# Kernel optimization log

Measured on AMD Instinct MI355X. Metric: run time of the kernel, lower is better.

## Reference

```python
import jax, jax.numpy as jnp
import numpy as np

T, D, H, HD = 2048, 2048, 16, 128
ROPE_BASE = 10000.0
NEG = jnp.float32(-1e30)


def rms_norm(x):
    # F.rms_norm(x, (x.size(-1),)) with default eps = dtype eps
    eps = jnp.finfo(x.dtype).eps
    return x * jax.lax.rsqrt(jnp.mean(x * x, axis=-1, keepdims=True) + eps)


def rotary(x):
    # x: [1, T, H, hd]; half-split rotation as in Rotary.forward
    hd = x.shape[-1]
    inv_freq = (1.0 / ROPE_BASE) ** (jnp.arange(0, hd, 2, dtype=jnp.float32) / hd)
    t = jnp.arange(x.shape[1], dtype=jnp.float32)
    freqs = jnp.outer(t, inv_freq)                      # [T, hd/2]
    cos = jnp.cos(freqs)[None, :, None, :]
    sin = jnp.sin(freqs)[None, :, None, :]
    x1, x2 = jnp.split(x, 2, axis=-1)
    return jnp.concatenate([x1 * cos + x2 * sin, -x1 * sin + x2 * cos], axis=-1)


def setup_inputs() -> dict:
    key = jax.random.key(0)
    ks = jax.random.split(key, 10)
    w = lambda k, shape: jax.random.normal(k, shape, jnp.float32) * 0.02
    return {
        "x":  jax.random.normal(ks[0], (1, T, D), jnp.float32),
        "vi": jax.random.normal(ks[1], (1, T, H, HD), jnp.float32),
        "x0": jax.random.normal(ks[2], (1, T, D), jnp.float32),
        "wq": w(ks[3], (D, D)),
        "wk": w(ks[4], (D, D)),
        "wv": w(ks[5], (D, D)),
        "wo": w(ks[6], (D, D)),
        "lamb": jnp.float32(0.5),
        "lambdas": jnp.array([1.0, 0.0], jnp.float32),
        "w_fc": w(ks[7], (4 * D, D)),
        "w_proj": w(ks[8], (D, 4 * D)),
    }


def reference(x, vi, x0, wq, wk, wv, wo, lamb, lambdas, w_fc, w_proj):
    # Block: residual blend with initial embedding x0
    xb = lambdas[0] * x + lambdas[1] * x0
    xn = rms_norm(xb)

    # --- CausalSelfAttention ---
    q = (xn @ wq.T).reshape(1, T, H, HD)
    k = (xn @ wk.T).reshape(1, T, H, HD)
    v = (xn @ wv.T).reshape(1, T, H, HD)
    v = (1.0 - lamb) * v + lamb * vi                     # value-embedding blend
    q = rotary(rms_norm(q))
    k = rotary(rms_norm(k))

    scale = 1.0 / jnp.sqrt(jnp.float32(HD))              # flex_attention default scale
    scores = jnp.einsum('bqhd,bkhd->bhqk', q, k) * scale # [1,H,T,T]
    causal = jnp.tril(jnp.ones((T, T), bool))
    scores = jnp.where(causal[None, None], scores, NEG)
    attn = jax.nn.softmax(scores, axis=-1)
    y = jnp.einsum('bhqk,bkhd->bqhd', attn, v).reshape(1, T, D)
    a = y @ wo.T                                         # attention output REPLACES x (no residual)

    # --- MLP with squared ReLU ---
    h = rms_norm(a) @ w_fc.T
    h = jnp.square(jax.nn.relu(h))
    out = a + h @ w_proj.T
    return out
```

## Files before the change

### kernel.cpp

```cpp
#include <hip/hip_runtime.h>
#include <hip/hip_bf16.h>

typedef __bf16 bf16;
typedef __bf16 bf16x8 __attribute__((ext_vector_type(8)));
typedef float f32x4 __attribute__((ext_vector_type(4)));
typedef unsigned int u32x4 __attribute__((ext_vector_type(4)));

#define DD 2048
#define DD2 4194304ull
#define G9_LDS 131072

__device__ __forceinline__ void glds16(const void* g, void* l) {
  __builtin_amdgcn_global_load_lds((const __attribute__((address_space(1))) void*)g,
                                   (__attribute__((address_space(3))) void*)l, 16, 0, 0);
}

__device__ __forceinline__ f32x4 mfma16(bf16x8 a, bf16x8 b, f32x4 c) {
  return __builtin_amdgcn_mfma_f32_16x16x32_bf16(a, b, c, 0, 0, 0);
}

__device__ __forceinline__ unsigned pk2(float lo, float hi) {
  unsigned short a = __builtin_bit_cast(unsigned short, (bf16)lo);
  unsigned short b = __builtin_bit_cast(unsigned short, (bf16)hi);
  return (unsigned)a | ((unsigned)b << 16);
}

__global__ __launch_bounds__(256) void cvt_seg(const float* __restrict__ s0, const float* __restrict__ s1,
                                               const float* __restrict__ s2, const float* __restrict__ s3,
                                               bf16* __restrict__ dst, int seglog, size_t total) {
  size_t i = ((size_t)blockIdx.x * 256 + threadIdx.x) * 16;
  const size_t stride = (size_t)gridDim.x * 256 * 16;
  for (; i < total; i += stride) {
    int seg = (int)(i >> seglog);
    const float* src = (seg == 0) ? s0 : (seg == 1) ? s1 : (seg == 2) ? s2 : s3;
    size_t loc = i - ((size_t)seg << seglog);
    float4 a0 = *(const float4*)(src + loc);
    float4 a1 = *(const float4*)(src + loc + 4);
    float4 a2 = *(const float4*)(src + loc + 8);
    float4 a3 = *(const float4*)(src + loc + 12);
    bf16x8 o0, o1;
    o0[0] = (bf16)a0.x; o0[1] = (bf16)a0.y; o0[2] = (bf16)a0.z; o0[3] = (bf16)a0.w;
    o0[4] = (bf16)a1.x; o0[5] = (bf16)a1.y; o0[6] = (bf16)a1.z; o0[7] = (bf16)a1.w;
    o1[0] = (bf16)a2.x; o1[1] = (bf16)a2.y; o1[2] = (bf16)a2.z; o1[3] = (bf16)a2.w;
    o1[4] = (bf16)a3.x; o1[5] = (bf16)a3.y; o1[6] = (bf16)a3.z; o1[7] = (bf16)a3.w;
    *(bf16x8*)(dst + i) = o0;
    *(bf16x8*)(dst + i + 8) = o1;
  }
}

template<bool BLEND>
__global__ __launch_bounds__(256) void prenorm_k(const float* __restrict__ x, const float* __restrict__ x0,
                                                 const float* __restrict__ lambdas, bf16* __restrict__ out) {
  const int t = blockIdx.x, tid = threadIdx.x;
  const float4* xr = (const float4*)(x + (size_t)t * DD);
  float4 a0 = xr[2 * tid], a1 = xr[2 * tid + 1];
  float v[8] = {a0.x, a0.y, a0.z, a0.w, a1.x, a1.y, a1.z, a1.w};
  if (BLEND) {
    const float l0 = lambdas[0], l1 = lambdas[1];
    const float4* yr = (const float4*)(x0 + (size_t)t * DD);
    float4 b0 = yr[2 * tid], b1 = yr[2 * tid + 1];
    float w[8] = {b0.x, b0.y, b0.z, b0.w, b1.x, b1.y, b1.z, b1.w};
#pragma unroll
    for (int i = 0; i < 8; ++i) v[i] = l0 * v[i] + l1 * w[i];
  }
  float ss = 0.f;
#pragma unroll
  for (int i = 0; i < 8; ++i) ss += v[i] * v[i];
#pragma unroll
  for (int off = 1; off < 64; off <<= 1) ss += __shfl_xor(ss, off, 64);
  __shared__ float red[4];
  const int wid = tid >> 6;
  if ((tid & 63) == 0) red[wid] = ss;
  __syncthreads();
  ss = red[0] + red[1] + red[2] + red[3];
  const float sc = rsqrtf(ss * (1.0f / DD) + 1.1920928955078125e-07f);
  bf16x8 o;
#pragma unroll
  for (int i = 0; i < 8; ++i) o[i] = (bf16)(v[i] * sc);
  *(bf16x8*)(out + (size_t)t * DD + tid * 8) = o;
}

__global__ __launch_bounds__(256) void rope_k(bf16* __restrict__ qg, bf16* __restrict__ kg) {
  const int tid = threadIdx.x, lane = tid & 63, wid = tid >> 6;
  const int p = blockIdx.x * 4 + wid;
  bf16* base = ((p >> 15) ? kg : qg);
  const int t = (p >> 4) & 2047, hh = p & 15;
  base += (size_t)t * DD + hh * 128;
  float x1 = (float)base[lane], x2 = (float)base[lane + 64];
  float ss = x1 * x1 + x2 * x2;
#pragma unroll
  for (int off = 1; off < 64; off <<= 1) ss += __shfl_xor(ss, off, 64);
  const float sc = rsqrtf(ss * (1.0f / 128.0f) + 1.1920928955078125e-07f);
  x1 *= sc; x2 *= sc;
  const float fr = (float)t * exp2f((float)lane * (-13.287712379549449f / 64.0f));
  const float s = sinf(fr), c = cosf(fr);
  base[lane]      = (bf16)(x1 * c + x2 * s);
  base[lane + 64] = (bf16)(-x1 * s + x2 * c);
}

__global__ __launch_bounds__(256) void vt_k(const bf16* __restrict__ v, bf16* __restrict__ vt) {
  __shared__ alignas(16) bf16 tile[16 * 128];
  const int tb = blockIdx.x, hb = blockIdx.y, tid = threadIdx.x;
  glds16(v + (size_t)(tb * 16 + (tid >> 4)) * DD + hb * 128 + (tid & 15) * 8, tile + tid * 8);
  __syncthreads();
  const int d_l = tid & 127, tc = tid >> 7;
  bf16x8 o;
#pragma unroll
  for (int i = 0; i < 8; ++i) o[i] = tile[(tc * 8 + i) * 128 + d_l];
  *(bf16x8*)(vt + (size_t)(hb * 128 + d_l) * DD + tb * 16 + tc * 8) = o;
}

__device__ __forceinline__ void g9_stageA(const bf16* A, int Kstride, int row0, int k0,
                                          bf16* buf, int hm, int tid) {
#pragma unroll
  for (int i = 0; i < 2; ++i) {
    int e = tid + i * 512;
    int prl = e >> 3, slot = e & 7;
    int wm = prl >> 6, r63 = prl & 63;
    glds16(A + (size_t)(row0 + wm * 128 + hm * 64 + r63) * Kstride + k0 + ((slot ^ (prl & 7)) * 8),
           buf + hm * 8192 + e * 8);
  }
}
__device__ __forceinline__ void g9_stageB(const bf16* B, int Kstride, int col0, int k0,
                                          bf16* buf, int hn, int tid) {
#pragma unroll
  for (int i = 0; i < 2; ++i) {
    int e = tid + i * 512;
    int pbl = e >> 3, slot = e & 7;
    int wn = pbl >> 5, q = pbl & 31;
    glds16(B + (size_t)(col0 + wn * 64 + hn * 32 + q) * Kstride + k0 + ((slot ^ (pbl & 7)) * 8),
           buf + 16384 + hn * 8192 + e * 8);
  }
}

__device__ __forceinline__ void gemm9_core(const bf16* __restrict__ A, const bf16* __restrict__ B,
                                           int Kstride, int Klen, int row0, int col0,
                                           bf16* smem, f32x4 (&acc)[8][4]) {
  const int tid = threadIdx.x, lane = tid & 63, wid = tid >> 6;
  const int wm = wid >> 2, wn = wid & 3;
  const int l15 = lane & 15, g = lane >> 4;
  const int sw = l15 & 7;
  const int NT = Klen >> 6;
  g9_stageA(A, Kstride, row0, 0, smem, 0, tid);
  g9_stageB(B, Kstride, col0, 0, smem, 0, tid);
  g9_stageB(B, Kstride, col0, 0, smem, 1, tid);
  g9_stageA(A, Kstride, row0, 0, smem, 1, tid);
  g9_stageA(A, Kstride, row0, 64, smem + 32768, 0, tid);
  g9_stageB(B, Kstride, col0, 64, smem + 32768, 0, tid);
  asm volatile("s_waitcnt vmcnt(8)" ::: "memory");
  __builtin_amdgcn_s_barrier();

  bf16x8 a[4][2], b0[2][2], b1[2][2];
  for (int t = 0; t < NT; ++t) {
    bf16* cb = smem + (t & 1) * 32768;
    bf16* nb = smem + ((t + 1) & 1) * 32768;
    const bool s1 = (t + 1) < NT, s2 = (t + 2) < NT;
#pragma unroll
    for (int mm = 0; mm < 4; ++mm)
#pragma unroll
      for (int ks = 0; ks < 2; ++ks)
        a[mm][ks] = *(const bf16x8*)(cb + (wm * 64 + mm * 16 + l15) * 64 + (((ks * 4 + g) ^ sw) * 8));
#pragma unroll
    for (int nn = 0; nn < 2; ++nn)
#pragma unroll
      for (int ks = 0; ks < 2; ++ks)
        b0[nn][ks] = *(const bf16x8*)(cb + 16384 + (wn * 32 + nn * 16 + l15) * 64 + (((ks * 4 + g) ^ sw) * 8));
    if (s1) { g9_stageB(B, Kstride, col0, (t + 1) << 6, nb, 1, tid);
              g9_stageA(A, Kstride, row0, (t + 1) << 6, nb, 1, tid);
              asm volatile("s_waitcnt vmcnt(8)" ::: "memory"); }
    else    { asm volatile("s_waitcnt vmcnt(0)" ::: "memory"); }
    __builtin_amdgcn_s_barrier();
    __builtin_amdgcn_s_setprio(1);
#pragma unroll
    for (int mm = 0; mm < 4; ++mm)
#pragma unroll
      for (int nn = 0; nn < 2; ++nn)
#pragma unroll
        for (int ks = 0; ks < 2; ++ks)
          acc[mm][nn] = mfma16(a[mm][ks], b0[nn][ks], acc[mm][nn]);
    __builtin_amdgcn_s_setprio(0);
#pragma unroll
    for (int nn = 0; nn < 2; ++nn)
#pragma unroll
      for (int ks = 0; ks < 2; ++ks)
        b1[nn][ks] = *(const bf16x8*)(cb + 16384 + 8192 + (wn * 32 + nn * 16 + l15) * 64 + (((ks * 4 + g) ^ sw) * 8));
    __builtin_amdgcn_s_barrier();
    __builtin_amdgcn_s_setprio(1);
#pragma unroll
    for (int mm = 0; mm < 4; ++mm)
#pragma unroll
      for (int nn = 0; nn < 2; ++nn)
#pragma unroll
        for (int ks = 0; ks < 2; ++ks)
          acc[mm][2 + nn] = mfma16(a[mm][ks], b1[nn][ks], acc[mm][2 + nn]);
    __builtin_amdgcn_s_setprio(0);
#pragma unroll
    for (int mm = 0; mm < 4; ++mm)
#pragma unroll
      for (int ks = 0; ks < 2; ++ks)
        a[mm][ks] = *(const bf16x8*)(cb + 8192 + (wm * 64 + mm * 16 + l15) * 64 + (((ks * 4 + g) ^ sw) * 8));
    __builtin_amdgcn_s_barrier();
    __builtin_amdgcn_s_setprio(1);
#pragma unroll
    for (int mm = 0; mm < 4; ++mm)
#pragma unroll
      for (int nn = 0; nn < 2; ++nn)
#pragma unroll
        for (int ks = 0; ks < 2; ++ks)
          acc[4 + mm][nn] = mfma16(a[mm][ks], b0[nn][ks], acc[4 + mm][nn]);
    __builtin_amdgcn_s_setprio(0);
    if (s2) { g9_stageA(A, Kstride, row0, (t + 2) << 6, cb, 0, tid);
              g9_stageB(B, Kstride, col0, (t + 2) << 6, cb, 0, tid);
              asm volatile("s_waitcnt vmcnt(8)" ::: "memory"); }
    else if (s1) { asm volatile("s_waitcnt vmcnt(4)" ::: "memory"); }
    __builtin_amdgcn_s_barrier();
    __builtin_amdgcn_s_setprio(1);
#pragma unroll
    for (int mm = 0; mm < 4; ++mm)
#pragma unroll
      for (int nn = 0; nn < 2; ++nn)
#pragma unroll
        for (int ks = 0; ks < 2; ++ks)
          acc[4 + mm][2 + nn] = mfma16(a[mm][ks], b1[nn][ks], acc[4 + mm][2 + nn]);
    __builtin_amdgcn_s_setprio(0);
  }
}

#define GEMM9_EPI(STMT)                                                        \
  { const int lane_ = threadIdx.x & 63, wid_ = threadIdx.x >> 6;               \
    const int l15_ = lane_ & 15, g_ = lane_ >> 4;                              \
    const int wm_ = wid_ >> 2, wn_ = wid_ & 3;                                 \
    _Pragma("unroll") for (int m = 0; m < 8; ++m)                              \
    _Pragma("unroll") for (int n = 0; n < 4; ++n)                              \
    _Pragma("unroll") for (int j = 0; j < 4; ++j) {                            \
      int grow = row0 + wm_ * 128 + (m >> 2) * 64 + (m & 3) * 16 + g_ * 4 + j; \
      int gcol = col0 + wn_ * 64 + (n >> 1) * 32 + (n & 1) * 16 + l15_;        \
      float vacc = acc[m][n][j];                                               \
      STMT; } }

__global__ __launch_bounds__(512, 1) void gemm9_qkv(const bf16* __restrict__ A,
    const bf16* __restrict__ Wq, const bf16* __restrict__ Wk, const bf16* __restrict__ Wv,
    bf16* __restrict__ oq, bf16* __restrict__ ok, bf16* __restrict__ ov,
    const float* __restrict__ vi, const float* __restrict__ lambp) {
  extern __shared__ bf16 smem9[];
  const int z = blockIdx.z;
  const bf16* B = (z == 0) ? Wq : (z == 1) ? Wk : Wv;
  bf16* out = (z == 0) ? oq : (z == 1) ? ok : ov;
  const int row0 = blockIdx.y * 256, col0 = blockIdx.x * 256;
  f32x4 acc[8][4] = {};
  gemm9_core(A, B, DD, DD, row0, col0, smem9, acc);
  if (z < 2) {
    GEMM9_EPI( out[(size_t)grow * DD + gcol] = (bf16)vacc; )
  } else {
    const float lam = *lambp;
    GEMM9_EPI( out[(size_t)grow * DD + gcol] =
                 (bf16)((1.0f - lam) * vacc + lam * vi[(size_t)grow * DD + gcol]); )
  }
}

__global__ __launch_bounds__(512, 1) void gemm9_part(const bf16* __restrict__ A, const bf16* __restrict__ B,
                                                     float* __restrict__ o1, float* __restrict__ o2,
                                                     int zsw, int N, int Kstride, int Klen) {
  extern __shared__ bf16 smem9[];
  const int row0 = blockIdx.y * 256, col0 = blockIdx.x * 256;
  const int z = blockIdx.z, kofs = z * Klen;
  float* out = (z < zsw) ? (o1 + (size_t)z * DD2) : (o2 + (size_t)(z - zsw) * DD2);
  f32x4 acc[8][4] = {};
  gemm9_core(A + kofs, B + kofs, Kstride, Klen, row0, col0, smem9, acc);
  GEMM9_EPI( out[(size_t)grow * N + gcol] = vacc; )
}

__global__ __launch_bounds__(512, 1) void gemm9_relu(const bf16* __restrict__ A, const bf16* __restrict__ B,
                                                     bf16* __restrict__ out, int N, int Kstride, int Klen) {
  extern __shared__ bf16 smem9[];
  const int row0 = blockIdx.y * 256, col0 = blockIdx.x * 256;
  f32x4 acc[8][4] = {};
  gemm9_core(A, B, Kstride, Klen, row0, col0, smem9, acc);
  GEMM9_EPI( float r = fmaxf(vacc, 0.f); out[(size_t)grow * N + gcol] = (bf16)(r * r); )
}

__global__ __launch_bounds__(256) void wo_red_prenorm(const float* __restrict__ pa, const float* __restrict__ pb,
                                                      float* __restrict__ a_f, bf16* __restrict__ an) {
  const int t = blockIdx.x, tid = threadIdx.x;
  const size_t base = (size_t)t * DD + tid * 8;
  float v[8];
#pragma unroll
  for (int h = 0; h < 2; ++h) {
    size_t i = base + h * 4;
    float4 r0 = *(const float4*)(pa + i);
    float4 r1 = *(const float4*)(pa + DD2 + i);
    float4 r2 = *(const float4*)(pb + i);
    float4 r3 = *(const float4*)(pb + DD2 + i);
    v[h*4+0] = r0.x + r1.x + r2.x + r3.x;
    v[h*4+1] = r0.y + r1.y + r2.y + r3.y;
    v[h*4+2] = r0.z + r1.z + r2.z + r3.z;
    v[h*4+3] = r0.w + r1.w + r2.w + r3.w;
  }
  *(float4*)(a_f + base)     = make_float4(v[0], v[1], v[2], v[3]);
  *(float4*)(a_f + base + 4) = make_float4(v[4], v[5], v[6], v[7]);
  float ss = 0.f;
#pragma unroll
  for (int i = 0; i < 8; ++i) ss += v[i] * v[i];
#pragma unroll
  for (int off = 1; off < 64; off <<= 1) ss += __shfl_xor(ss, off, 64);
  __shared__ float red[4];
  if ((tid & 63) == 0) red[tid >> 6] = ss;
  __syncthreads();
  ss = red[0] + red[1] + red[2] + red[3];
  const float sc = rsqrtf(ss * (1.0f / DD) + 1.1920928955078125e-07f);
  bf16x8 o;
#pragma unroll
  for (int i = 0; i < 8; ++i) o[i] = (bf16)(v[i] * sc);
  *(bf16x8*)(an + base) = o;
}

__global__ __launch_bounds__(256) void proj_red(const float* __restrict__ pa, const float* __restrict__ pw,
                                                const float* __restrict__ a_f, float* __restrict__ out) {
  const size_t base = ((size_t)blockIdx.x * 256 + threadIdx.x) * 8;
#pragma unroll
  for (int h = 0; h < 2; ++h) {
    size_t i = base + h * 4;
    float4 r = *(const float4*)(a_f + i);
    float4 u = *(const float4*)(pa + i);
    float4 w = *(const float4*)(pa + DD2 + i);
    float4 z = *(const float4*)(pa + 2 * DD2 + i);
    float4 y = *(const float4*)(pw + i);
    *(float4*)(out + i) = make_float4(r.x + u.x + w.x + z.x + y.x,
                                      r.y + u.y + w.y + z.y + y.y,
                                      r.z + u.z + w.z + z.z + y.z,
                                      r.w + u.w + w.w + z.w + y.w);
  }
}

__device__ __forceinline__ void att_stageK(const bf16* kg, int h, int kt, bf16* dst, int tid) {
#pragma unroll
  for (int r = 0; r < 2; ++r) {
    int e = tid + r * 256, row = e >> 4, slot = e & 15;
    glds16(kg + (size_t)(kt * 32 + row) * DD + h * 128 + ((slot ^ (row & 7)) * 8), dst + e * 8);
  }
}
__device__ __forceinline__ void att_stageV(const bf16* vtg, int h, int kt, bf16* dst, int tid) {
#pragma unroll
  for (int r = 0; r < 2; ++r) {
    int e = tid + r * 256, d = e >> 2, slot = e & 3;
    glds16(vtg + (size_t)(h * 128 + d) * DD + kt * 32 + ((slot ^ ((d >> 1) & 3)) * 8), dst + e * 8);
  }
}

__global__ __launch_bounds__(256) void attn_k(const bf16* __restrict__ qg, const bf16* __restrict__ kg,
                                              const bf16* __restrict__ vtg, bf16* __restrict__ yg) {
  __shared__ alignas(16) bf16 Ks[3][32 * 128];
  __shared__ alignas(16) bf16 Vt[3][128 * 32];
  const int h = blockIdx.y, qb = 31 - blockIdx.x;
  const int tid = threadIdx.x, lane = tid & 63, wid = tid >> 6;
  const int l15 = lane & 15, g = lane >> 4, swl = l15 & 7;
  const int qrow = qb * 64 + wid * 16;
  const float scale = 0.08838834764831845f;
  bf16x8 aQ[4];
  {
    const bf16* qp = qg + (size_t)(qrow + l15) * DD + h * 128 + g * 8;
#pragma unroll
    for (int kc = 0; kc < 4; ++kc) aQ[kc] = *(const bf16x8*)(qp + kc * 32);
  }
  f32x4 acc[8] = {};
  float lsum = 0.f;
  const int nkt = qb * 2 + 2;
  att_stageK(kg, h, 0, Ks[0], tid);
  att_stageV(vtg, h, 0, Vt[0], tid);
  att_stageK(kg, h, 1, Ks[1], tid);
  att_stageV(vtg, h, 1, Vt[1], tid);
  asm volatile("s_waitcnt vmcnt(4)" ::: "memory");
  __builtin_amdgcn_s_barrier();
  int cur = 0;
  for (int kt = 0; kt < nkt; ++kt) {
    const int kbase = kt * 32;
    const int nb = (cur >= 1) ? cur - 1 : 2;
    bf16x8 kf0[4], kf1[4];
#pragma unroll
    for (int kc = 0; kc < 4; ++kc) {
      kf0[kc] = *(const bf16x8*)(Ks[cur] + l15 * 128 + (((kc * 4 + g) ^ swl) * 8));
      kf1[kc] = *(const bf16x8*)(Ks[cur] + (16 + l15) * 128 + (((kc * 4 + g) ^ swl) * 8));
    }
    if (kt + 2 < nkt) { att_stageK(kg, h, kt + 2, Ks[nb], tid);
                        att_stageV(vtg, h, kt + 2, Vt[nb], tid); }
    f32x4 S0 = {}, S1 = {};
#pragma unroll
    for (int kc = 0; kc < 4; ++kc) {
      S0 = mfma16(kf0[kc], aQ[kc], S0);
      S1 = mfma16(kf1[kc], aQ[kc], S1);
    }
    const int q = qrow + l15;
    float p0[4], p1[4];
#pragma unroll
    for (int j = 0; j < 4; ++j) {
      int k0 = kbase + 4 * g + j;
      p0[j] = (k0 <= q) ? __expf(S0[j] * scale) : 0.f;
      p1[j] = (k0 + 16 <= q) ? __expf(S1[j] * scale) : 0.f;
      lsum += p0[j] + p1[j];
    }
    unsigned w0 = pk2(p0[0], p0[1]), w1 = pk2(p0[2], p0[3]);
    unsigned w2 = pk2(p1[0], p1[1]), w3 = pk2(p1[2], p1[3]);
    const int s0l = (g & 1) * 32 + l15, s1l = s0l + 16;
    const bool hi = g >= 2;
    unsigned t00 = __shfl(w0, s0l, 64), t10 = __shfl(w1, s0l, 64);
    unsigned t01 = __shfl(w0, s1l, 64), t11 = __shfl(w1, s1l, 64);
    unsigned u00 = __shfl(w2, s0l, 64), u10 = __shfl(w3, s0l, 64);
    unsigned u01 = __shfl(w2, s1l, 64), u11 = __shfl(w3, s1l, 64);
    u32x4 av = { hi ? u00 : t00, hi ? u10 : t10, hi ? u01 : t01, hi ? u11 : t11 };
    bf16x8 aP = __builtin_bit_cast(bf16x8, av);
#pragma unroll
    for (int dt = 0; dt < 8; ++dt) {
      int d = dt * 16 + l15;
      bf16x8 bV = *(const bf16x8*)(Vt[cur] + d * 32 + ((g ^ ((d >> 1) & 3)) * 8));
      acc[dt] = mfma16(aP, bV, acc[dt]);
    }
    if (kt + 1 < nkt) {
      if (kt + 2 < nkt) { asm volatile("s_waitcnt vmcnt(4)" ::: "memory"); }
      else              { asm volatile("s_waitcnt vmcnt(0)" ::: "memory"); }
      __builtin_amdgcn_s_barrier();
    }
    cur = (cur == 2) ? 0 : cur + 1;
  }
  lsum += __shfl_xor(lsum, 16, 64);
  lsum += __shfl_xor(lsum, 32, 64);
  f32x4 linv;
#pragma unroll
  for (int j = 0; j < 4; ++j) linv[j] = 1.0f / __shfl(lsum, 4 * g + j, 64);
#pragma unroll
  for (int dt = 0; dt < 8; ++dt)
#pragma unroll
    for (int j = 0; j < 4; ++j) {
      int q = qrow + 4 * g + j;
      yg[(size_t)q * DD + h * 128 + dt * 16 + l15] = (bf16)(acc[dt][j] * linv[j]);
    }
}

extern "C" void kernel_launch(void* const* d_in, const int* in_sizes, int n_in,
                              void* d_out, int out_size, void* d_ws, size_t ws_size,
                              hipStream_t stream) {
  const float* x       = (const float*)d_in[0];
  const float* vi      = (const float*)d_in[1];
  const float* x0      = (const float*)d_in[2];
  const float* wq      = (const float*)d_in[3];
  const float* wk      = (const float*)d_in[4];
  const float* wv      = (const float*)d_in[5];
  const float* wo      = (const float*)d_in[6];
  const float* lamb    = (const float*)d_in[7];
  const float* lambdas = (const float*)d_in[8];
  const float* wfc     = (const float*)d_in[9];
  const float* wproj   = (const float*)d_in[10];
  float* out = (float*)d_out;

  (void)hipFuncSetAttribute(reinterpret_cast<const void*>(gemm9_qkv),
                            hipFuncAttributeMaxDynamicSharedMemorySize, G9_LDS);
  (void)hipFuncSetAttribute(reinterpret_cast<const void*>(gemm9_part),
                            hipFuncAttributeMaxDynamicSharedMemorySize, G9_LDS);
  (void)hipFuncSetAttribute(reinterpret_cast<const void*>(gemm9_relu),
                            hipFuncAttributeMaxDynamicSharedMemorySize, G9_LDS);

  char* wsb = (char*)d_ws;
  size_t off = 0;
  auto alloc = [&](size_t bytes) { void* p = wsb + off; off = (off + bytes + 255) & ~(size_t)255; return p; };
  bf16* wq_b  = (bf16*)alloc(DD2 * 2);
  bf16* wk_b  = (bf16*)alloc(DD2 * 2);
  bf16* wv_b  = (bf16*)alloc(DD2 * 2);
  bf16* wo_b  = (bf16*)alloc(DD2 * 2);
  bf16* wfc_b = (bf16*)alloc(DD2 * 8);
  bf16* wpj_b = (bf16*)alloc(DD2 * 8);
  bf16* xn_b  = (bf16*)alloc(DD2 * 2);
  bf16* q_b   = (bf16*)alloc(DD2 * 2);
  bf16* k_b   = (bf16*)alloc(DD2 * 2);
  bf16* v_b   = (bf16*)alloc(DD2 * 2);
  bf16* y_b   = (bf16*)alloc(DD2 * 2);
  bf16* an_b  = (bf16*)alloc(DD2 * 2);
  float* partA = (float*)xn_b;
  float* a_f  = (float*)alloc(DD2 * 4);
  bf16* h_b   = (bf16*)alloc(DD2 * 8);
  bf16* vt_b  = h_b;
  float* partB = (float*)h_b;

  cvt_seg<<<2048, 256, 0, stream>>>(wq, wk, wv, wo, (bf16*)wsb, 22, 4 * DD2);
  prenorm_k<true><<<2048, 256, 0, stream>>>(x, x0, lambdas, xn_b);
  gemm9_qkv<<<dim3(8, 8, 3), 512, G9_LDS, stream>>>(xn_b, wq_b, wk_b, wv_b, q_b, k_b, v_b, vi, lamb);
  rope_k<<<16384, 256, 0, stream>>>(q_b, k_b);
  vt_k<<<dim3(128, 16), 256, 0, stream>>>(v_b, vt_b);
  attn_k<<<dim3(32, 16), 256, 0, stream>>>(q_b, k_b, vt_b, y_b);
  gemm9_part<<<dim3(8, 8, 4), 512, G9_LDS, stream>>>(y_b, wo_b, partA, partB, 2, DD, DD, 512);
  wo_red_prenorm<<<2048, 256, 0, stream>>>(partA, partB, a_f, an_b);
  cvt_seg<<<2048, 256, 0, stream>>>(wfc, wproj, wfc, wfc, wfc_b, 24, 8 * DD2);
  gemm9_relu<<<dim3(32, 8), 512, G9_LDS, stream>>>(an_b, wfc_b, h_b, 4 * DD, DD, DD);
  gemm9_part<<<dim3(8, 8, 4), 512, G9_LDS, stream>>>(h_b, wpj_b, partA, (float*)wfc_b, 3, DD, 4 * DD, 2048);
  proj_red<<<2048, 256, 0, stream>>>(partA, (float*)wfc_b, a_f, out);
}
```

Measured before the change: 386.6 us.

## Restructure GEMM main loop into two-stage unrolled pipeline with finer-grained staging

Rewrites the bf16 GEMM core loop so both LDS buffers are fully prefetched up front and the loop is unrolled by two over buffer halves. Global-to-LDS loads for tile t+2 are split into four quarter stages interleaved between MFMA phases, and explicit lgkmcnt waits replace implicit ones. The aim is to hide global load latency and spread memory traffic across the compute phases. It adds more barriers per tile and assumes NT is even, and the waitcnt arithmetic is fragile.

```diff
diff --git a/kernel.cpp b/kernel.cpp
--- a/kernel.cpp
+++ b/kernel.cpp
@@ -147,82 +147,94 @@
   g9_stageA(A, Kstride, row0, 0, smem, 1, tid);
   g9_stageA(A, Kstride, row0, 64, smem + 32768, 0, tid);
   g9_stageB(B, Kstride, col0, 64, smem + 32768, 0, tid);
+  g9_stageB(B, Kstride, col0, 64, smem + 32768, 1, tid);
+  g9_stageA(A, Kstride, row0, 64, smem + 32768, 1, tid);
   asm volatile("s_waitcnt vmcnt(8)" ::: "memory");
   __builtin_amdgcn_s_barrier();
 
   bf16x8 a[4][2], b0[2][2], b1[2][2];
-  for (int t = 0; t < NT; ++t) {
-    bf16* cb = smem + (t & 1) * 32768;
-    bf16* nb = smem + ((t + 1) & 1) * 32768;
-    const bool s1 = (t + 1) < NT, s2 = (t + 2) < NT;
-#pragma unroll
-    for (int mm = 0; mm < 4; ++mm)
-#pragma unroll
-      for (int ks = 0; ks < 2; ++ks)
-        a[mm][ks] = *(const bf16x8*)(cb + (wm * 64 + mm * 16 + l15) * 64 + (((ks * 4 + g) ^ sw) * 8));
-#pragma unroll
-    for (int nn = 0; nn < 2; ++nn)
-#pragma unroll
-      for (int ks = 0; ks < 2; ++ks)
-        b0[nn][ks] = *(const bf16x8*)(cb + 16384 + (wn * 32 + nn * 16 + l15) * 64 + (((ks * 4 + g) ^ sw) * 8));
-    if (s1) { g9_stageB(B, Kstride, col0, (t + 1) << 6, nb, 1, tid);
-              g9_stageA(A, Kstride, row0, (t + 1) << 6, nb, 1, tid);
-              asm volatile("s_waitcnt vmcnt(8)" ::: "memory"); }
-    else    { asm volatile("s_waitcnt vmcnt(0)" ::: "memory"); }
-    __builtin_amdgcn_s_barrier();
-    __builtin_amdgcn_s_setprio(1);
-#pragma unroll
-    for (int mm = 0; mm < 4; ++mm)
+  const int NI = NT >> 1;
+  for (int i = 0; i < NI; ++i) {
+#pragma unroll
+    for (int h = 0; h < 2; ++h) {
+      bf16* cb = smem + h * 32768;
+      const int kst = (2 * i + 2 + h) << 6;
+      const bool st = (2 * i + 2 + h) < NT;
+#pragma unroll
+      for (int mm = 0; mm < 4; ++mm)
+#pragma unroll
+        for (int ks = 0; ks < 2; ++ks)
+          a[mm][ks] = *(const bf16x8*)(cb + (wm * 64 + mm * 16 + l15) * 64 + (((ks * 4 + g) ^ sw) * 8));
 #pragma unroll
       for (int nn = 0; nn < 2; ++nn)
 #pragma unroll
         for (int ks = 0; ks < 2; ++ks)
-          acc[mm][nn] = mfma16(a[mm][ks], b0[nn][ks], acc[mm][nn]);
-    __builtin_amdgcn_s_setprio(0);
-#pragma unroll
-    for (int nn = 0; nn < 2; ++nn)
-#pragma unroll
-      for (int ks = 0; ks < 2; ++ks)
-        b1[nn][ks] = *(const bf16x8*)(cb + 16384 + 8192 + (wn * 32 + nn * 16 + l15) * 64 + (((ks * 4 + g) ^ sw) * 8));
-    __builtin_amdgcn_s_barrier();
-    __builtin_amdgcn_s_setprio(1);
-#pragma unroll
-    for (int mm = 0; mm < 4; ++mm)
+          b0[nn][ks] = *(const bf16x8*)(cb + 16384 + (wn * 32 + nn * 16 + l15) * 64 + (((ks * 4 + g) ^ sw) * 8));
+      asm volatile("s_waitcnt lgkmcnt(8)" ::: "memory");
+      __builtin_amdgcn_s_barrier();
+      asm volatile("s_waitcnt lgkmcnt(0)" ::: "memory");
+      __builtin_amdgcn_s_setprio(1);
+#pragma unroll
+      for (int mm = 0; mm < 4; ++mm)
+#pragma unroll
+        for (int nn = 0; nn < 2; ++nn)
+#pragma unroll
+          for (int ks = 0; ks < 2; ++ks)
+            acc[mm][nn] = mfma16(a[mm][ks], b0[nn][ks], acc[mm][nn]);
+      __builtin_amdgcn_s_setprio(0);
+      __builtin_amdgcn_s_barrier();
 #pragma unroll
       for (int nn = 0; nn < 2; ++nn)
 #pragma unroll
         for (int ks = 0; ks < 2; ++ks)
-          acc[mm][2 + nn] = mfma16(a[mm][ks], b1[nn][ks], acc[mm][2 + nn]);
-    __builtin_amdgcn_s_setprio(0);
-#pragma unroll
-    for (int mm = 0; mm < 4; ++mm)
-#pragma unroll
-      for (int ks = 0; ks < 2; ++ks)
-        a[mm][ks] = *(const bf16x8*)(cb + 8192 + (wm * 64 + mm * 16 + l15) * 64 + (((ks * 4 + g) ^ sw) * 8));
-    __builtin_amdgcn_s_barrier();
-    __builtin_amdgcn_s_setprio(1);
-#pragma unroll
-    for (int mm = 0; mm < 4; ++mm)
-#pragma unroll
-      for (int nn = 0; nn < 2; ++nn)
+          b1[nn][ks] = *(const bf16x8*)(cb + 16384 + 8192 + (wn * 32 + nn * 16 + l15) * 64 + (((ks * 4 + g) ^ sw) * 8));
+      if (st) { g9_stageA(A, Kstride, row0, kst, cb, 0, tid);
+                g9_stageB(B, Kstride, col0, kst, cb, 0, tid); }
+      __builtin_amdgcn_s_barrier();
+      asm volatile("s_waitcnt lgkmcnt(0)" ::: "memory");
+      __builtin_amdgcn_s_setprio(1);
+#pragma unroll
+      for (int mm = 0; mm < 4; ++mm)
+#pragma unroll
+        for (int nn = 0; nn < 2; ++nn)
+#pragma unroll
+          for (int ks = 0; ks < 2; ++ks)
+            acc[mm][2 + nn] = mfma16(a[mm][ks], b1[nn][ks], acc[mm][2 + nn]);
+      __builtin_amdgcn_s_setprio(0);
+      __builtin_amdgcn_s_barrier();
+#pragma unroll
+      for (int mm = 0; mm < 4; ++mm)
 #pragma unroll
         for (int ks = 0; ks < 2; ++ks)
-          acc[4 + mm][nn] = mfma16(a[mm][ks], b0[nn][ks], acc[4 + mm][nn]);
-    __builtin_amdgcn_s_setprio(0);
-    if (s2) { g9_stageA(A, Kstride, row0, (t + 2) << 6, cb, 0, tid);
-              g9_stageB(B, Kstride, col0, (t + 2) << 6, cb, 0, tid);
-              asm volatile("s_waitcnt vmcnt(8)" ::: "memory"); }
-    else if (s1) { asm volatile("s_waitcnt vmcnt(4)" ::: "memory"); }
-    __builtin_amdgcn_s_barrier();
-    __builtin_amdgcn_s_setprio(1);
-#pragma unroll
-    for (int mm = 0; mm < 4; ++mm)
-#pragma unroll
-      for (int nn = 0; nn < 2; ++nn)
-#pragma unroll
-        for (int ks = 0; ks < 2; ++ks)
-          acc[4 + mm][2 + nn] = mfma16(a[mm][ks], b1[nn][ks], acc[4 + mm][2 + nn]);
-    __builtin_amdgcn_s_setprio(0);
+          a[mm][ks] = *(const bf16x8*)(cb + 8192 + (wm * 64 + mm * 16 + l15) * 64 + (((ks * 4 + g) ^ sw) * 8));
+      if (st) g9_stageB(B, Kstride, col0, kst, cb, 1, tid);
+      __builtin_amdgcn_s_barrier();
+      asm volatile("s_waitcnt lgkmcnt(0)" ::: "memory");
+      __builtin_amdgcn_s_setprio(1);
+#pragma unroll
+      for (int mm = 0; mm < 4; ++mm)
+#pragma unroll
+        for (int nn = 0; nn < 2; ++nn)
+#pragma unroll
+          for (int ks = 0; ks < 2; ++ks)
+            acc[4 + mm][nn] = mfma16(a[mm][ks], b0[nn][ks], acc[4 + mm][nn]);
+      __builtin_amdgcn_s_setprio(0);
+      __builtin_amdgcn_s_barrier();
+      if (st) g9_stageA(A, Kstride, row0, kst, cb, 1, tid);
+      __builtin_amdgcn_s_barrier();
+      __builtin_amdgcn_s_setprio(1);
+#pragma unroll
+      for (int mm = 0; mm < 4; ++mm)
+#pragma unroll
+        for (int nn = 0; nn < 2; ++nn)
+#pragma unroll
+          for (int ks = 0; ks < 2; ++ks)
+            acc[4 + mm][2 + nn] = mfma16(a[mm][ks], b1[nn][ks], acc[4 + mm][2 + nn]);
+      __builtin_amdgcn_s_setprio(0);
+      if (st) { asm volatile("s_waitcnt vmcnt(8)" ::: "memory"); }
+      else    { asm volatile("s_waitcnt vmcnt(0)" ::: "memory"); }
+      __builtin_amdgcn_s_barrier();
+    }
   }
 }
 
```

New measurement: 450.8 us. 16.6% more time.
